# Kernel optimization log

Measured on AMD Instinct MI355X. Metric: run time of the kernel, lower is better.

Reference implementation:

```python
import jax, jax.numpy as jnp
import numpy as np

C = 128   # channels
C4 = C // 4

def setup_inputs() -> dict:
    key = jax.random.key(0)
    k1, k2, k3, k4, k5 = jax.random.split(key, 5)
    B, N = 16, 2048
    x_h = jax.random.normal(k1, (B, C, N), dtype=jnp.float32)
    x_o = jax.random.normal(k2, (B, C, N), dtype=jnp.float32)
    # q_conv and k_conv share the SAME weight (tied in __init__), bias=False
    w_qk = jax.random.normal(k3, (C4, C), dtype=jnp.float32) * (1.0 / np.sqrt(C))
    # v_conv: Conv1d(C, C, 1) with bias
    w_v = jax.random.normal(k4, (C, C), dtype=jnp.float32) * (1.0 / np.sqrt(C))
    b_v = jax.random.normal(k5, (C,), dtype=jnp.float32) * 0.01
    return {"x_h": x_h, "x_o": x_o, "w_qk": w_qk, "w_v": w_v, "b_v": b_v}

def reference(x_h, x_o, w_qk, w_v, b_v):
    # SA_Layer_1 forward (only layer used by Grasp_Transformer_Last.forward)
    # 1x1 conv == channel matmul
    xh_q = jnp.einsum('dc,bcn->bnd', w_qk, x_h)            # [B, Nh, C4]
    xo_k = jnp.einsum('dc,bcm->bdm', w_qk, x_o)            # [B, C4, No]
    alpha = jnp.einsum('bnd,bdm->bnm', xh_q, xo_k)         # [B, Nh, No]
    # no softmax: normalize by column sums over dim=1 (Nh axis)
    attention = alpha / (1e-9 + jnp.sum(alpha, axis=1, keepdims=True))
    xo_v = jnp.einsum('dc,bcm->bmd', w_v, x_o) + b_v       # [B, No, C]
    x_r = jnp.einsum('bnm,bmd->bnd', attention, xo_v)      # [B, Nh, C]
    x_r = jnp.transpose(x_r, (0, 2, 1))                    # [B, C, Nh]
    return (x_r, attention)
```

## Files before the change

### kernel.cpp

```cpp
#include <hip/hip_runtime.h>

constexpr int NTOK = 2048;
constexpr int CH   = 128;
constexpr int C4   = 32;
constexpr int NB   = 16;

typedef __attribute__((ext_vector_type(8))) __bf16 bf16x8;
typedef __attribute__((ext_vector_type(4))) float  f32x4;

__device__ __forceinline__ unsigned short f2bf(float f) {
  union { float f; unsigned u; } v; v.f = f;
  unsigned r = v.u + 0x7fffu + ((v.u >> 16) & 1u);
  return (unsigned short)(r >> 16);
}
__device__ __forceinline__ float bf2f(unsigned short h) {
  union { unsigned u; float f; } v; v.u = ((unsigned)h) << 16;
  return v.f;
}

__global__ __launch_bounds__(256) void rs_kernel(const float* __restrict__ x_h,
                                                 double* __restrict__ rowsumH) {
  const int t = threadIdx.x;
  const int c0 = blockIdx.x * 16;
  const int b = blockIdx.y;
  __shared__ double red[4];
  for (int cl = 0; cl < 16; ++cl) {
    const float* rp = x_h + (size_t)(b * CH + c0 + cl) * NTOK;
    double s = 0.0;
    for (int i = 0; i < 2; ++i) {
      float4 v = *(const float4*)(rp + (t + 256 * i) * 4);
      s += (double)v.x + (double)v.y + (double)v.z + (double)v.w;
    }
    for (int off = 1; off <= 32; off <<= 1) s += __shfl_xor(s, off);
    if ((t & 63) == 0) red[t >> 6] = s;
    __syncthreads();
    if (t == 0) rowsumH[b * CH + c0 + cl] = red[0] + red[1] + red[2] + red[3];
    __syncthreads();
  }
}

__global__ __launch_bounds__(256) void p_kernel(const double* __restrict__ rowsumH,
                                                const float* __restrict__ w_qk,
                                                double* __restrict__ P) {
  const int t = threadIdx.x, b = blockIdx.x;
  __shared__ double Sl[C4];
  if (t < C4) {
    double s = 0.0;
    for (int c = 0; c < CH; ++c) s += (double)w_qk[t * CH + c] * rowsumH[b * CH + c];
    Sl[t] = s;
  }
  __syncthreads();
  if (t < CH) {
    double p = 0.0;
    for (int d = 0; d < C4; ++d) p += Sl[d] * (double)w_qk[d * CH + t];
    P[b * CH + t] = p;
  }
}

__global__ __launch_bounds__(256) void prep_qk(const float* __restrict__ x_h,
                                               const float* __restrict__ x_o,
                                               const float* __restrict__ w_qk,
                                               float* __restrict__ xhq_f32,
                                               float* __restrict__ xokT_f32,
                                               unsigned short* __restrict__ xhq_hi,
                                               unsigned short* __restrict__ xokT_hi,
                                               unsigned short* __restrict__ xhq_lo,
                                               unsigned short* __restrict__ xokT_lo) {
  const int t = threadIdx.x;
  const int n0 = blockIdx.x * 64;
  const int b = blockIdx.y;
  const int which = blockIdx.z;
  const float* src = which ? x_o : x_h;
  float* dstf = which ? xokT_f32 : xhq_f32;
  unsigned short* dsth = which ? xokT_hi : xhq_hi;
  unsigned short* dstl = which ? xokT_lo : xhq_lo;

  __shared__ float Xt[CH][64];
  __shared__ float Wl[C4][132];

  for (int i = 0; i < 8; ++i) {
    int flat = t + 256 * i;
    int c = flat >> 4, f4 = flat & 15;
    float4 v = *(const float4*)(src + (size_t)(b * CH + c) * NTOK + n0 + f4 * 4);
    *(float4*)&Xt[c][f4 * 4] = v;
  }
  for (int i = 0; i < 4; ++i) {
    int flat = t + 256 * i;
    int d = flat >> 5, f4 = flat & 31;
    float4 v = *(const float4*)(w_qk + d * CH + f4 * 4);
    *(float4*)&Wl[d][f4 * 4] = v;
  }
  __syncthreads();

  const int nb = (t & 15) * 4;
  const int d0 = (t >> 4) * 2;
  float acc[4][2] = {};
#pragma unroll 4
  for (int c = 0; c < CH; ++c) {
    float4 x4 = *(const float4*)&Xt[c][nb];
    float w0 = Wl[d0][c], w1 = Wl[d0 + 1][c];
    acc[0][0] += x4.x * w0; acc[0][1] += x4.x * w1;
    acc[1][0] += x4.y * w0; acc[1][1] += x4.y * w1;
    acc[2][0] += x4.z * w0; acc[2][1] += x4.z * w1;
    acc[3][0] += x4.w * w0; acc[3][1] += x4.w * w1;
  }

  const size_t robase = (size_t)(b * NTOK + n0 + nb);
#pragma unroll
  for (int i = 0; i < 4; ++i) {
    size_t base = (robase + i) * C4 + d0;
    *(float2*)(dstf + base) = make_float2(acc[i][0], acc[i][1]);
    unsigned short h0 = f2bf(acc[i][0]), h1 = f2bf(acc[i][1]);
    *(unsigned*)(dsth + base) = (unsigned)h0 | ((unsigned)h1 << 16);
    unsigned short l0 = f2bf(acc[i][0] - bf2f(h0));
    unsigned short l1 = f2bf(acc[i][1] - bf2f(h1));
    *(unsigned*)(dstl + base) = (unsigned)l0 | ((unsigned)l1 << 16);
  }
}

__global__ __launch_bounds__(256) void inv_s2(const float* __restrict__ x_o,
                                              const double* __restrict__ P,
                                              const float* __restrict__ xokT_f32,
                                              float* __restrict__ inv,
                                              float* __restrict__ S2) {
  const int t = threadIdx.x;
  const int b = blockIdx.y;
  const int m = blockIdx.x * 256 + t;
  __shared__ double Pl[CH];
  __shared__ float S2l[C4];
  if (t < CH) Pl[t] = P[b * CH + t];
  if (t < C4) S2l[t] = 0.f;
  __syncthreads();
  double cs = 0.0;
  const float* xp = x_o + (size_t)b * CH * NTOK + m;
#pragma unroll 8
  for (int c = 0; c < CH; ++c) cs += Pl[c] * (double)xp[(size_t)c * NTOK];
  float iv = (float)(1.0 / (1e-9 + cs));
  inv[b * NTOK + m] = iv;
  const float* rp = xokT_f32 + (size_t)(b * NTOK + m) * C4;
  for (int dd = 0; dd < C4; ++dd) {
    int d2 = (dd + t) & 31;
    atomicAdd(&S2l[d2], rp[d2] * iv);
  }
  __syncthreads();
  if (t < C4) atomicAdd(&S2[b * C4 + t], S2l[t]);
}

__global__ __launch_bounds__(256) void u_kernel(const float* __restrict__ x_o,
                                                const float* __restrict__ xokT_f32,
                                                const float* __restrict__ inv,
                                                float* __restrict__ U) {
  const int t = threadIdx.x;
  const int c0 = blockIdx.x * 8;
  const int mbase0 = blockIdx.y * 512;
  const int b = blockIdx.z;
  const int d = t & 31, cl = t >> 5;
  __shared__ float Xs[8][256];
  float acc = 0.f;
  for (int cc = 0; cc < 2; ++cc) {
    const int mb = mbase0 + cc * 256;
    __syncthreads();
    for (int i = 0; i < 2; ++i) {
      int flat = t + 256 * i;
      int row = flat >> 6, f4 = flat & 63;
      float4 xv = *(const float4*)(x_o + (size_t)(b * CH + c0 + row) * NTOK + mb + f4 * 4);
      float4 iv = *(const float4*)(inv + b * NTOK + mb + f4 * 4);
      xv.x *= iv.x; xv.y *= iv.y; xv.z *= iv.z; xv.w *= iv.w;
      *(float4*)&Xs[row][f4 * 4] = xv;
    }
    __syncthreads();
    const float* ap = xokT_f32 + (size_t)(b * NTOK + mb) * C4 + d;
#pragma unroll 4
    for (int mm = 0; mm < 256; mm += 4) {
      float4 xq = *(const float4*)&Xs[cl][mm];
      float a0 = ap[(mm + 0) * C4];
      float a1 = ap[(mm + 1) * C4];
      float a2 = ap[(mm + 2) * C4];
      float a3 = ap[(mm + 3) * C4];
      acc += a0 * xq.x + a1 * xq.y + a2 * xq.z + a3 * xq.w;
    }
  }
  atomicAdd(&U[(size_t)(b * C4 + d) * CH + c0 + cl], acc);
}

__global__ __launch_bounds__(256) void t_kernel(const float* __restrict__ U,
                                                const float* __restrict__ w_v,
                                                const float* __restrict__ b_v,
                                                const float* __restrict__ S2,
                                                float* __restrict__ T) {
  const int t = threadIdx.x, b = blockIdx.x;
  __shared__ float Wl[CH * CH];
  for (int i = 0; i < 16; ++i) {
    int flat = t + 256 * i;
    *(float4*)&Wl[flat * 4] = *(const float4*)(w_v + flat * 4);
  }
  __syncthreads();
  const int d = t & 31;
  const int cg = (t >> 5) * 16;
  float acc[16] = {};
  const float* up = U + (size_t)(b * C4 + d) * CH;
  for (int cp = 0; cp < CH; ++cp) {
    float u = up[cp];
#pragma unroll
    for (int j = 0; j < 16; ++j) acc[j] += u * Wl[(cg + j) * CH + cp];
  }
  float s2 = S2[b * C4 + d];
#pragma unroll
  for (int j = 0; j < 16; ++j) acc[j] += s2 * b_v[cg + j];
  float* tp = T + (size_t)(b * C4 + d) * CH + cg;
#pragma unroll
  for (int j = 0; j < 16; j += 4)
    *(float4*)(tp + j) = make_float4(acc[j], acc[j + 1], acc[j + 2], acc[j + 3]);
}

__global__ __launch_bounds__(256) void xr_kernel(const float* __restrict__ xhq_f32,
                                                 const float* __restrict__ T,
                                                 float* __restrict__ out0) {
  const int t = threadIdx.x;
  const int n = blockIdx.x * 256 + t;
  const int b = blockIdx.y;
  __shared__ float Tl[CH][36];
  for (int i = 0; i < 16; ++i) {
    int flat = t + 256 * i;
    int d = flat >> 7, c = flat & 127;
    Tl[c][d] = T[(size_t)b * C4 * CH + flat];
  }
  __syncthreads();
  float xq[C4];
  const float* qp = xhq_f32 + (size_t)(b * NTOK + n) * C4;
#pragma unroll
  for (int i = 0; i < 8; ++i) {
    float4 v = *(const float4*)(qp + i * 4);
    xq[i * 4] = v.x; xq[i * 4 + 1] = v.y; xq[i * 4 + 2] = v.z; xq[i * 4 + 3] = v.w;
  }
  float* op = out0 + (size_t)b * CH * NTOK + n;
  for (int c = 0; c < CH; ++c) {
    float acc = 0.f;
#pragma unroll
    for (int dd = 0; dd < C4; dd += 4) {
      float4 tv = *(const float4*)&Tl[c][dd];
      acc += xq[dd] * tv.x + xq[dd + 1] * tv.y + xq[dd + 2] * tv.z + xq[dd + 3] * tv.w;
    }
    op[(size_t)c * NTOK] = acc;
  }
}

__global__ __launch_bounds__(256) void attn_kernel(const unsigned short* __restrict__ xhq_hi,
                                                   const unsigned short* __restrict__ xhq_lo,
                                                   const unsigned short* __restrict__ xokT_hi,
                                                   const unsigned short* __restrict__ xokT_lo,
                                                   const float* __restrict__ inv,
                                                   float* __restrict__ out1) {
  const int t = threadIdx.x;
  const int wave = t >> 6, lane = t & 63;
  const int quad = lane >> 4, l16 = lane & 15;
  const int m0 = blockIdx.x * 64;
  const int n0 = blockIdx.y * 64;
  const int b = blockIdx.z;

  const int n = n0 + wave * 16 + l16;
  const size_t abase = (size_t)(b * NTOK + n) * C4 + quad * 8;
  bf16x8 ah = *(const bf16x8*)(const void*)(xhq_hi + abase);
  bf16x8 al = *(const bf16x8*)(const void*)(xhq_lo + abase);

  bf16x8 bh[4], bl[4];
  float invv[4];
#pragma unroll
  for (int tt = 0; tt < 4; ++tt) {
    int m = m0 + tt * 16 + l16;
    size_t bbase = (size_t)(b * NTOK + m) * C4 + quad * 8;
    bh[tt] = *(const bf16x8*)(const void*)(xokT_hi + bbase);
    bl[tt] = *(const bf16x8*)(const void*)(xokT_lo + bbase);
    invv[tt] = inv[b * NTOK + m];
  }

  const int nrow = n0 + wave * 16 + quad * 4;
#pragma unroll
  for (int tt = 0; tt < 4; ++tt) {
    f32x4 z = {0.f, 0.f, 0.f, 0.f};
    f32x4 acc = __builtin_amdgcn_mfma_f32_16x16x32_bf16(al, bh[tt], z, 0, 0, 0);
    acc = __builtin_amdgcn_mfma_f32_16x16x32_bf16(ah, bl[tt], acc, 0, 0, 0);
    acc = __builtin_amdgcn_mfma_f32_16x16x32_bf16(ah, bh[tt], acc, 0, 0, 0);
#pragma unroll
    for (int r = 0; r < 4; ++r) {
      float v = acc[r] * invv[tt];
      size_t off = ((size_t)(b * NTOK) + nrow + r) * NTOK + m0 + tt * 16 + l16;
      __builtin_nontemporal_store(v, out1 + off);
    }
  }
}

extern "C" void kernel_launch(void* const* d_in, const int* in_sizes, int n_in,
                              void* d_out, int out_size, void* d_ws, size_t ws_size,
                              hipStream_t stream) {
  (void)in_sizes; (void)n_in; (void)out_size; (void)ws_size;
  const float* x_h  = (const float*)d_in[0];
  const float* x_o  = (const float*)d_in[1];
  const float* w_qk = (const float*)d_in[2];
  const float* w_v  = (const float*)d_in[3];
  const float* b_v  = (const float*)d_in[4];
  float* out0 = (float*)d_out;
  float* out1 = out0 + (size_t)NB * CH * NTOK;

  char* ws = (char*)d_ws;
  float* xhq_f32        = (float*)(ws + 0);
  float* xokT_f32       = (float*)(ws + 4194304);
  unsigned short* xhq_hi  = (unsigned short*)(ws + 8388608);
  unsigned short* xokT_hi = (unsigned short*)(ws + 10485760);
  unsigned short* xhq_lo  = (unsigned short*)(ws + 12582912);
  unsigned short* xokT_lo = (unsigned short*)(ws + 14680064);
  float* inv      = (float*)(ws + 16777216);
  float* S2       = (float*)(ws + 16908288);
  float* U        = (float*)(ws + 16910336);
  float* T        = (float*)(ws + 17172480);
  double* rowsumH = (double*)(ws + 17434624);
  double* P       = (double*)(ws + 17450880);

  hipMemsetAsync(S2, 0, 2048 + 262144, stream);

  rs_kernel <<<dim3(8, NB), 256, 0, stream>>>(x_h, rowsumH);
  p_kernel  <<<NB, 256, 0, stream>>>(rowsumH, w_qk, P);
  prep_qk   <<<dim3(32, NB, 2), 256, 0, stream>>>(x_h, x_o, w_qk, xhq_f32, xokT_f32,
                                                  xhq_hi, xokT_hi, xhq_lo, xokT_lo);
  inv_s2    <<<dim3(8, NB), 256, 0, stream>>>(x_o, P, xokT_f32, inv, S2);
  u_kernel  <<<dim3(16, 4, NB), 256, 0, stream>>>(x_o, xokT_f32, inv, U);
  t_kernel  <<<NB, 256, 0, stream>>>(U, w_v, b_v, S2, T);
  xr_kernel <<<dim3(8, NB), 256, 0, stream>>>(xhq_f32, T, out0);
  attn_kernel<<<dim3(32, 32, NB), 256, 0, stream>>>(xhq_hi, xhq_lo, xokT_hi, xokT_lo,
                                                    inv, out1);
}
```

Measured before the change: 446.6 us.

## Stage attention output through LDS for vector stores and retile prep/xr kernels

The attention kernel now stages each 64x64 MFMA result tile in shared memory, then writes it with 16-byte nontemporal stores, and each block loops over four column tiles. This replaces scattered scalar stores to the 256MB attention output. prep_qk is retiled to 256 tokens x 8 outputs per thread, and it no longer writes an fp32 copy of xhq. xr_kernel rebuilds xhq from the hi/lo bf16 pair, handles two tokens per thread and reads a transposed T. rs_kernel gives each row to one 32-lane group and drops the shared-memory reduction, at the cost of extra LDS traffic and synchronisation in the attention kernel.

```diff
diff --git a/kernel.cpp b/kernel.cpp
--- a/kernel.cpp
+++ b/kernel.cpp
@@ -7,6 +7,7 @@
 
 typedef __attribute__((ext_vector_type(8))) __bf16 bf16x8;
 typedef __attribute__((ext_vector_type(4))) float  f32x4;
+typedef __attribute__((ext_vector_type(8))) unsigned short us8;
 
 __device__ __forceinline__ unsigned short f2bf(float f) {
   union { float f; unsigned u; } v; v.f = f;
@@ -21,22 +22,18 @@
 __global__ __launch_bounds__(256) void rs_kernel(const float* __restrict__ x_h,
                                                  double* __restrict__ rowsumH) {
   const int t = threadIdx.x;
-  const int c0 = blockIdx.x * 16;
+  const int ch = t >> 5, lane = t & 31;
+  const int c = blockIdx.x * 8 + ch;
   const int b = blockIdx.y;
-  __shared__ double red[4];
-  for (int cl = 0; cl < 16; ++cl) {
-    const float* rp = x_h + (size_t)(b * CH + c0 + cl) * NTOK;
-    double s = 0.0;
-    for (int i = 0; i < 2; ++i) {
-      float4 v = *(const float4*)(rp + (t + 256 * i) * 4);
-      s += (double)v.x + (double)v.y + (double)v.z + (double)v.w;
-    }
-    for (int off = 1; off <= 32; off <<= 1) s += __shfl_xor(s, off);
-    if ((t & 63) == 0) red[t >> 6] = s;
-    __syncthreads();
-    if (t == 0) rowsumH[b * CH + c0 + cl] = red[0] + red[1] + red[2] + red[3];
-    __syncthreads();
-  }
+  const float* rp = x_h + (size_t)(b * CH + c) * NTOK;
+  double s = 0.0;
+#pragma unroll
+  for (int i = 0; i < 16; ++i) {
+    float4 v = *(const float4*)(rp + (lane + 32 * i) * 4);
+    s += (double)v.x + (double)v.y + (double)v.z + (double)v.w;
+  }
+  for (int off = 1; off <= 16; off <<= 1) s += __shfl_xor(s, off);
+  if (lane == 0) rowsumH[b * CH + c] = s;
 }
 
 __global__ __launch_bounds__(256) void p_kernel(const double* __restrict__ rowsumH,
@@ -60,61 +57,79 @@
 __global__ __launch_bounds__(256) void prep_qk(const float* __restrict__ x_h,
                                                const float* __restrict__ x_o,
                                                const float* __restrict__ w_qk,
-                                               float* __restrict__ xhq_f32,
-                                               float* __restrict__ xokT_f32,
                                                unsigned short* __restrict__ xhq_hi,
+                                               unsigned short* __restrict__ xhq_lo,
                                                unsigned short* __restrict__ xokT_hi,
-                                               unsigned short* __restrict__ xhq_lo,
-                                               unsigned short* __restrict__ xokT_lo) {
-  const int t = threadIdx.x;
-  const int n0 = blockIdx.x * 64;
+                                               unsigned short* __restrict__ xokT_lo,
+                                               float* __restrict__ xokT_f32) {
+  const int t = threadIdx.x;
+  const int n0 = blockIdx.x * 256;
   const int b = blockIdx.y;
   const int which = blockIdx.z;
   const float* src = which ? x_o : x_h;
-  float* dstf = which ? xokT_f32 : xhq_f32;
   unsigned short* dsth = which ? xokT_hi : xhq_hi;
   unsigned short* dstl = which ? xokT_lo : xhq_lo;
 
-  __shared__ float Xt[CH][64];
-  __shared__ float Wl[C4][132];
-
-  for (int i = 0; i < 8; ++i) {
-    int flat = t + 256 * i;
-    int c = flat >> 4, f4 = flat & 15;
-    float4 v = *(const float4*)(src + (size_t)(b * CH + c) * NTOK + n0 + f4 * 4);
-    *(float4*)&Xt[c][f4 * 4] = v;
-  }
+  __shared__ float Xt[32 * 256];
+  __shared__ float Wt[CH * 36];
+
   for (int i = 0; i < 4; ++i) {
-    int flat = t + 256 * i;
-    int d = flat >> 5, f4 = flat & 31;
-    float4 v = *(const float4*)(w_qk + d * CH + f4 * 4);
-    *(float4*)&Wl[d][f4 * 4] = v;
-  }
-  __syncthreads();
-
-  const int nb = (t & 15) * 4;
-  const int d0 = (t >> 4) * 2;
-  float acc[4][2] = {};
+    int flat4 = t + 256 * i;
+    int d = flat4 >> 5, c4 = (flat4 & 31) * 4;
+    float4 v = *(const float4*)(w_qk + d * CH + c4);
+    Wt[(c4 + 0) * 36 + d] = v.x;
+    Wt[(c4 + 1) * 36 + d] = v.y;
+    Wt[(c4 + 2) * 36 + d] = v.z;
+    Wt[(c4 + 3) * 36 + d] = v.w;
+  }
+
+  const int ng = t & 63;
+  const int d0 = (t >> 6) * 8;
+  float acc[4][8] = {};
+
+  for (int cc = 0; cc < 4; ++cc) {
+    __syncthreads();
+    for (int i = 0; i < 8; ++i) {
+      int flat4 = t + 256 * i;
+      int row = flat4 >> 6, n4 = flat4 & 63;
+      float4 v = *(const float4*)(src + (size_t)(b * CH + cc * 32 + row) * NTOK + n0 + n4 * 4);
+      *(float4*)&Xt[row * 256 + n4 * 4] = v;
+    }
+    __syncthreads();
 #pragma unroll 4
-  for (int c = 0; c < CH; ++c) {
-    float4 x4 = *(const float4*)&Xt[c][nb];
-    float w0 = Wl[d0][c], w1 = Wl[d0 + 1][c];
-    acc[0][0] += x4.x * w0; acc[0][1] += x4.x * w1;
-    acc[1][0] += x4.y * w0; acc[1][1] += x4.y * w1;
-    acc[2][0] += x4.z * w0; acc[2][1] += x4.z * w1;
-    acc[3][0] += x4.w * w0; acc[3][1] += x4.w * w1;
-  }
-
-  const size_t robase = (size_t)(b * NTOK + n0 + nb);
-#pragma unroll
-  for (int i = 0; i < 4; ++i) {
-    size_t base = (robase + i) * C4 + d0;
-    *(float2*)(dstf + base) = make_float2(acc[i][0], acc[i][1]);
-    unsigned short h0 = f2bf(acc[i][0]), h1 = f2bf(acc[i][1]);
-    *(unsigned*)(dsth + base) = (unsigned)h0 | ((unsigned)h1 << 16);
-    unsigned short l0 = f2bf(acc[i][0] - bf2f(h0));
-    unsigned short l1 = f2bf(acc[i][1] - bf2f(h1));
-    *(unsigned*)(dstl + base) = (unsigned)l0 | ((unsigned)l1 << 16);
+    for (int c64 = 0; c64 < 32; ++c64) {
+      const int c = cc * 32 + c64;
+      float4 x4 = *(const float4*)&Xt[c64 * 256 + ng * 4];
+      float4 wa = *(const float4*)&Wt[c * 36 + d0];
+      float4 wb = *(const float4*)&Wt[c * 36 + d0 + 4];
+      acc[0][0] += x4.x * wa.x; acc[0][1] += x4.x * wa.y; acc[0][2] += x4.x * wa.z; acc[0][3] += x4.x * wa.w;
+      acc[0][4] += x4.x * wb.x; acc[0][5] += x4.x * wb.y; acc[0][6] += x4.x * wb.z; acc[0][7] += x4.x * wb.w;
+      acc[1][0] += x4.y * wa.x; acc[1][1] += x4.y * wa.y; acc[1][2] += x4.y * wa.z; acc[1][3] += x4.y * wa.w;
+      acc[1][4] += x4.y * wb.x; acc[1][5] += x4.y * wb.y; acc[1][6] += x4.y * wb.z; acc[1][7] += x4.y * wb.w;
+      acc[2][0] += x4.z * wa.x; acc[2][1] += x4.z * wa.y; acc[2][2] += x4.z * wa.z; acc[2][3] += x4.z * wa.w;
+      acc[2][4] += x4.z * wb.x; acc[2][5] += x4.z * wb.y; acc[2][6] += x4.z * wb.z; acc[2][7] += x4.z * wb.w;
+      acc[3][0] += x4.w * wa.x; acc[3][1] += x4.w * wa.y; acc[3][2] += x4.w * wa.z; acc[3][3] += x4.w * wa.w;
+      acc[3][4] += x4.w * wb.x; acc[3][5] += x4.w * wb.y; acc[3][6] += x4.w * wb.z; acc[3][7] += x4.w * wb.w;
+    }
+  }
+
+#pragma unroll
+  for (int j = 0; j < 4; ++j) {
+    const int n = n0 + ng * 4 + j;
+    const size_t base = (size_t)(b * NTOK + n) * C4 + d0;
+    us8 hv, lv;
+#pragma unroll
+    for (int k = 0; k < 8; ++k) {
+      unsigned short h = f2bf(acc[j][k]);
+      hv[k] = h;
+      lv[k] = f2bf(acc[j][k] - bf2f(h));
+    }
+    *(us8*)(dsth + base) = hv;
+    *(us8*)(dstl + base) = lv;
+    if (which) {
+      *(float4*)(xokT_f32 + base) = make_float4(acc[j][0], acc[j][1], acc[j][2], acc[j][3]);
+      *(float4*)(xokT_f32 + base + 4) = make_float4(acc[j][4], acc[j][5], acc[j][6], acc[j][7]);
+    }
   }
 }
 
@@ -187,7 +202,7 @@
                                                 const float* __restrict__ w_v,
                                                 const float* __restrict__ b_v,
                                                 const float* __restrict__ S2,
-                                                float* __restrict__ T) {
+                                                float* __restrict__ T2) {
   const int t = threadIdx.x, b = blockIdx.x;
   __shared__ float Wl[CH * CH];
   for (int i = 0; i < 16; ++i) {
@@ -206,42 +221,56 @@
   }
   float s2 = S2[b * C4 + d];
 #pragma unroll
-  for (int j = 0; j < 16; ++j) acc[j] += s2 * b_v[cg + j];
-  float* tp = T + (size_t)(b * C4 + d) * CH + cg;
-#pragma unroll
-  for (int j = 0; j < 16; j += 4)
-    *(float4*)(tp + j) = make_float4(acc[j], acc[j + 1], acc[j + 2], acc[j + 3]);
-}
-
-__global__ __launch_bounds__(256) void xr_kernel(const float* __restrict__ xhq_f32,
-                                                 const float* __restrict__ T,
+  for (int j = 0; j < 16; ++j) {
+    acc[j] += s2 * b_v[cg + j];
+    T2[(size_t)(b * CH + cg + j) * C4 + d] = acc[j];
+  }
+}
+
+__global__ __launch_bounds__(256) void xr_kernel(const unsigned short* __restrict__ xhq_hi,
+                                                 const unsigned short* __restrict__ xhq_lo,
+                                                 const float* __restrict__ T2,
                                                  float* __restrict__ out0) {
   const int t = threadIdx.x;
-  const int n = blockIdx.x * 256 + t;
+  const int n0 = blockIdx.x * 128;
   const int b = blockIdx.y;
-  __shared__ float Tl[CH][36];
-  for (int i = 0; i < 16; ++i) {
-    int flat = t + 256 * i;
-    int d = flat >> 7, c = flat & 127;
-    Tl[c][d] = T[(size_t)b * C4 * CH + flat];
-  }
-  __syncthreads();
-  float xq[C4];
-  const float* qp = xhq_f32 + (size_t)(b * NTOK + n) * C4;
-#pragma unroll
-  for (int i = 0; i < 8; ++i) {
-    float4 v = *(const float4*)(qp + i * 4);
-    xq[i * 4] = v.x; xq[i * 4 + 1] = v.y; xq[i * 4 + 2] = v.z; xq[i * 4 + 3] = v.w;
-  }
-  float* op = out0 + (size_t)b * CH * NTOK + n;
-  for (int c = 0; c < CH; ++c) {
-    float acc = 0.f;
+  __shared__ float Tl[CH * 36];
+  for (int i = 0; i < 4; ++i) {
+    int flat4 = t + 256 * i;
+    int c = flat4 >> 3, dg = (flat4 & 7) * 4;
+    float4 v = *(const float4*)(T2 + (size_t)(b * CH + c) * C4 + dg);
+    *(float4*)&Tl[c * 36 + dg] = v;
+  }
+  __syncthreads();
+
+  const int na = n0 + (t & 63);
+  const int nb2 = na + 64;
+  const int cg = (t >> 6) * 32;
+
+  float qa[C4], qb[C4];
+#pragma unroll
+  for (int i = 0; i < 4; ++i) {
+    us8 h = *(const us8*)(xhq_hi + (size_t)(b * NTOK + na) * C4 + i * 8);
+    us8 l = *(const us8*)(xhq_lo + (size_t)(b * NTOK + na) * C4 + i * 8);
+#pragma unroll
+    for (int j = 0; j < 8; ++j) qa[i * 8 + j] = bf2f(h[j]) + bf2f(l[j]);
+    us8 h2 = *(const us8*)(xhq_hi + (size_t)(b * NTOK + nb2) * C4 + i * 8);
+    us8 l2 = *(const us8*)(xhq_lo + (size_t)(b * NTOK + nb2) * C4 + i * 8);
+#pragma unroll
+    for (int j = 0; j < 8; ++j) qb[i * 8 + j] = bf2f(h2[j]) + bf2f(l2[j]);
+  }
+
+  float* op = out0 + (size_t)b * CH * NTOK;
+  for (int c = cg; c < cg + 32; ++c) {
+    float acc1 = 0.f, acc2 = 0.f;
 #pragma unroll
     for (int dd = 0; dd < C4; dd += 4) {
-      float4 tv = *(const float4*)&Tl[c][dd];
-      acc += xq[dd] * tv.x + xq[dd + 1] * tv.y + xq[dd + 2] * tv.z + xq[dd + 3] * tv.w;
-    }
-    op[(size_t)c * NTOK] = acc;
+      float4 tv = *(const float4*)&Tl[c * 36 + dd];
+      acc1 += qa[dd] * tv.x + qa[dd + 1] * tv.y + qa[dd + 2] * tv.z + qa[dd + 3] * tv.w;
+      acc2 += qb[dd] * tv.x + qb[dd + 1] * tv.y + qb[dd + 2] * tv.z + qb[dd + 3] * tv.w;
+    }
+    op[(size_t)c * NTOK + na] = acc1;
+    op[(size_t)c * NTOK + nb2] = acc2;
   }
 }
 
@@ -254,39 +283,49 @@
   const int t = threadIdx.x;
   const int wave = t >> 6, lane = t & 63;
   const int quad = lane >> 4, l16 = lane & 15;
-  const int m0 = blockIdx.x * 64;
+  const int m00 = blockIdx.x * 256;
   const int n0 = blockIdx.y * 64;
   const int b = blockIdx.z;
 
+  __shared__ float Cs[64 * 68];
+
   const int n = n0 + wave * 16 + l16;
   const size_t abase = (size_t)(b * NTOK + n) * C4 + quad * 8;
-  bf16x8 ah = *(const bf16x8*)(const void*)(xhq_hi + abase);
-  bf16x8 al = *(const bf16x8*)(const void*)(xhq_lo + abase);
-
-  bf16x8 bh[4], bl[4];
-  float invv[4];
-#pragma unroll
-  for (int tt = 0; tt < 4; ++tt) {
-    int m = m0 + tt * 16 + l16;
-    size_t bbase = (size_t)(b * NTOK + m) * C4 + quad * 8;
-    bh[tt] = *(const bf16x8*)(const void*)(xokT_hi + bbase);
-    bl[tt] = *(const bf16x8*)(const void*)(xokT_lo + bbase);
-    invv[tt] = inv[b * NTOK + m];
-  }
-
-  const int nrow = n0 + wave * 16 + quad * 4;
-#pragma unroll
-  for (int tt = 0; tt < 4; ++tt) {
-    f32x4 z = {0.f, 0.f, 0.f, 0.f};
-    f32x4 acc = __builtin_amdgcn_mfma_f32_16x16x32_bf16(al, bh[tt], z, 0, 0, 0);
-    acc = __builtin_amdgcn_mfma_f32_16x16x32_bf16(ah, bl[tt], acc, 0, 0, 0);
-    acc = __builtin_amdgcn_mfma_f32_16x16x32_bf16(ah, bh[tt], acc, 0, 0, 0);
-#pragma unroll
-    for (int r = 0; r < 4; ++r) {
-      float v = acc[r] * invv[tt];
-      size_t off = ((size_t)(b * NTOK) + nrow + r) * NTOK + m0 + tt * 16 + l16;
-      __builtin_nontemporal_store(v, out1 + off);
-    }
+  const bf16x8 ah = *(const bf16x8*)(const void*)(xhq_hi + abase);
+  const bf16x8 al = *(const bf16x8*)(const void*)(xhq_lo + abase);
+
+  const int srow = t >> 2, scg = t & 3;
+
+  for (int mt = 0; mt < 4; ++mt) {
+    const int m0 = m00 + mt * 64;
+    bf16x8 bh[4], bl[4];
+    float invv[4];
+#pragma unroll
+    for (int tt = 0; tt < 4; ++tt) {
+      int m = m0 + tt * 16 + l16;
+      size_t bbase = (size_t)(b * NTOK + m) * C4 + quad * 8;
+      bh[tt] = *(const bf16x8*)(const void*)(xokT_hi + bbase);
+      bl[tt] = *(const bf16x8*)(const void*)(xokT_lo + bbase);
+      invv[tt] = inv[b * NTOK + m];
+    }
+#pragma unroll
+    for (int tt = 0; tt < 4; ++tt) {
+      f32x4 z = {0.f, 0.f, 0.f, 0.f};
+      f32x4 acc = __builtin_amdgcn_mfma_f32_16x16x32_bf16(al, bh[tt], z, 0, 0, 0);
+      acc = __builtin_amdgcn_mfma_f32_16x16x32_bf16(ah, bl[tt], acc, 0, 0, 0);
+      acc = __builtin_amdgcn_mfma_f32_16x16x32_bf16(ah, bh[tt], acc, 0, 0, 0);
+#pragma unroll
+      for (int r = 0; r < 4; ++r)
+        Cs[(wave * 16 + quad * 4 + r) * 68 + tt * 16 + l16] = acc[r] * invv[tt];
+    }
+    __syncthreads();
+#pragma unroll
+    for (int k = 0; k < 4; ++k) {
+      f32x4 v = *(const f32x4*)&Cs[srow * 68 + scg * 16 + k * 4];
+      size_t off = ((size_t)(b * NTOK) + n0 + srow) * NTOK + m0 + scg * 16 + k * 4;
+      __builtin_nontemporal_store(v, (f32x4*)(out1 + off));
+    }
+    __syncthreads();
   }
 }
 
@@ -303,29 +342,28 @@
   float* out1 = out0 + (size_t)NB * CH * NTOK;
 
   char* ws = (char*)d_ws;
-  float* xhq_f32        = (float*)(ws + 0);
-  float* xokT_f32       = (float*)(ws + 4194304);
-  unsigned short* xhq_hi  = (unsigned short*)(ws + 8388608);
-  unsigned short* xokT_hi = (unsigned short*)(ws + 10485760);
-  unsigned short* xhq_lo  = (unsigned short*)(ws + 12582912);
-  unsigned short* xokT_lo = (unsigned short*)(ws + 14680064);
-  float* inv      = (float*)(ws + 16777216);
-  float* S2       = (float*)(ws + 16908288);
-  float* U        = (float*)(ws + 16910336);
-  float* T        = (float*)(ws + 17172480);
-  double* rowsumH = (double*)(ws + 17434624);
-  double* P       = (double*)(ws + 17450880);
-
-  hipMemsetAsync(S2, 0, 2048 + 262144, stream);
-
-  rs_kernel <<<dim3(8, NB), 256, 0, stream>>>(x_h, rowsumH);
+  unsigned short* xhq_hi  = (unsigned short*)(ws + 0);
+  unsigned short* xhq_lo  = (unsigned short*)(ws + 2097152);
+  unsigned short* xokT_hi = (unsigned short*)(ws + 4194304);
+  unsigned short* xokT_lo = (unsigned short*)(ws + 6291456);
+  float* xokT_f32 = (float*)(ws + 8388608);
+  float* inv      = (float*)(ws + 12582912);
+  float* S2       = (float*)(ws + 12713984);
+  float* U        = (float*)(ws + 12716032);
+  float* T2       = (float*)(ws + 12978176);
+  double* rowsumH = (double*)(ws + 13240320);
+  double* P       = (double*)(ws + 13256704);
+
+  (void)hipMemsetAsync(S2, 0, 2048 + 262144, stream);
+
+  rs_kernel <<<dim3(16, NB), 256, 0, stream>>>(x_h, rowsumH);
   p_kernel  <<<NB, 256, 0, stream>>>(rowsumH, w_qk, P);
-  prep_qk   <<<dim3(32, NB, 2), 256, 0, stream>>>(x_h, x_o, w_qk, xhq_f32, xokT_f32,
-                                                  xhq_hi, xokT_hi, xhq_lo, xokT_lo);
+  prep_qk   <<<dim3(8, NB, 2), 256, 0, stream>>>(x_h, x_o, w_qk, xhq_hi, xhq_lo,
+                                                 xokT_hi, xokT_lo, xokT_f32);
   inv_s2    <<<dim3(8, NB), 256, 0, stream>>>(x_o, P, xokT_f32, inv, S2);
   u_kernel  <<<dim3(16, 4, NB), 256, 0, stream>>>(x_o, xokT_f32, inv, U);
-  t_kernel  <<<NB, 256, 0, stream>>>(U, w_v, b_v, S2, T);
-  xr_kernel <<<dim3(8, NB), 256, 0, stream>>>(xhq_f32, T, out0);
-  attn_kernel<<<dim3(32, 32, NB), 256, 0, stream>>>(xhq_hi, xhq_lo, xokT_hi, xokT_lo,
-                                                    inv, out1);
-}
+  t_kernel  <<<NB, 256, 0, stream>>>(U, w_v, b_v, S2, T2);
+  xr_kernel <<<dim3(16, NB), 256, 0, stream>>>(xhq_hi, xhq_lo, T2, out0);
+  attn_kernel<<<dim3(8, 32, NB), 256, 0, stream>>>(xhq_hi, xhq_lo, xokT_hi, xokT_lo,
+                                                   inv, out1);
+}
```

Result: slower. 746.1 us (+67.1%).
